# Optimization experiments

Hardware: AMD Instinct MI355X
Metric: run time of the kernel (lower is better)

The kernel has to match this reference:

```python
import jax, jax.numpy as jnp
import numpy as np
from jax.scipy.special import logsumexp

B, T, F = 32, 256, 32   # batch, line width (time), line height (features)
HID = 128
VOCAB = 100             # blank index = VOCAB
LBL = 32                # label length
NEG = -1e30


def _mdlstm(x, Wx, Wh1, Wh2, b):
    # x: [B, H, W, C] -> 2D LSTM: outer scan over width, inner scan over height
    Bb, H, W, C = x.shape
    hid = Wh1.shape[0]

    def col_step(carry, x_col):
        c_left, h_left = carry  # [H, B, hid] states from previous column

        def row_step(rc, inp):
            c_up, h_up = rc          # [B, hid] from previous row
            x_ij, c_l, h_l = inp     # [B, C], [B, hid], [B, hid]
            z = x_ij @ Wx + h_l @ Wh1 + h_up @ Wh2 + b  # [B, 5*hid]
            i_, g_, f1, f2, o_ = jnp.split(z, 5, axis=-1)
            c = jax.nn.sigmoid(f1) * c_l + jax.nn.sigmoid(f2) * c_up + jax.nn.sigmoid(i_) * jnp.tanh(g_)
            h = jax.nn.sigmoid(o_) * jnp.tanh(c)
            return (c, h), (c, h)

        z0 = jnp.zeros((Bb, hid), x.dtype)
        _, (c_col, h_col) = jax.lax.scan(row_step, (z0, z0), (x_col, c_left, h_left))
        return (c_col, h_col), h_col

    x_t = jnp.transpose(x, (2, 1, 0, 3))  # [W, H, B, C]
    zc = jnp.zeros((H, Bb, hid), x.dtype)
    _, hs = jax.lax.scan(col_step, (zc, zc), x_t)  # [W, H, B, hid]
    return jnp.transpose(hs, (2, 1, 0, 3))  # [B, H, W, hid]


def _ctc_loss(logp, labels, blank):
    # logp: [B, T, V] log-softmax; labels: [B, L] int in [0, blank)
    Bb, Tt, V = logp.shape
    Ll = labels.shape[1]
    S = 2 * Ll + 1
    ext = jnp.full((Bb, S), blank, dtype=labels.dtype).at[:, 1::2].set(labels)  # blank-interleaved
    lp_ext = jnp.take_along_axis(logp, jnp.broadcast_to(ext[:, None, :], (Bb, Tt, S)), axis=2)  # [B,T,S]
    prev2 = jnp.concatenate([jnp.full((Bb, 2), blank, dtype=ext.dtype), ext[:, :-2]], axis=1)
    skip = (ext != blank) & (ext != prev2)
    skip = skip.at[:, :2].set(False)
    alpha0 = jnp.full((Bb, S), NEG, logp.dtype).at[:, 0].set(lp_ext[:, 0, 0]).at[:, 1].set(lp_ext[:, 0, 1])

    def step(alpha, lp_t):
        a1 = jnp.concatenate([jnp.full((Bb, 1), NEG, alpha.dtype), alpha[:, :-1]], axis=1)
        a2 = jnp.concatenate([jnp.full((Bb, 2), NEG, alpha.dtype), alpha[:, :-2]], axis=1)
        a2 = jnp.where(skip, a2, NEG)
        new = logsumexp(jnp.stack([alpha, a1, a2], axis=0), axis=0) + lp_t
        return new, None

    alphaT, _ = jax.lax.scan(step, alpha0, jnp.transpose(lp_ext, (1, 0, 2))[1:])
    ll = logsumexp(jnp.stack([alphaT[:, -1], alphaT[:, -2]], axis=0), axis=0)
    return -ll  # [B]


def setup_inputs() -> dict:
    key = jax.random.key(0)
    ks = jax.random.split(key, 8)
    s = 0.08
    return {
        "X": jax.random.normal(ks[0], (B, T, F), jnp.float32),
        "y": jax.random.randint(ks[1], (B, LBL), 0, VOCAB),
        "Wx": jax.random.normal(ks[2], (1, 5 * HID), jnp.float32) * s,
        "Wh1": jax.random.normal(ks[3], (HID, 5 * HID), jnp.float32) * s,
        "Wh2": jax.random.normal(ks[4], (HID, 5 * HID), jnp.float32) * s,
        "b": jax.random.normal(ks[5], (5 * HID,), jnp.float32) * 0.01,
        "W_fc": jax.random.normal(ks[6], (HID, VOCAB + 1), jnp.float32) * s,
        "b_fc": jax.random.normal(ks[7], (VOCAB + 1,), jnp.float32) * 0.01,
    }


def reference(X, y, Wx, Wh1, Wh2, b, W_fc, b_fc):
    x = jnp.transpose(X, (0, 2, 1))[..., None]        # [B, F, T, 1] (image)
    h = _mdlstm(x, Wx, Wh1, Wh2, b)                    # [B, F, T, HID]
    feat = jnp.sum(h, axis=1)                          # collapse over height -> [B, T, HID]
    logits = feat @ W_fc + b_fc                        # [B, T, VOCAB+1]
    logp = jax.nn.log_softmax(logits, axis=-1)
    return _ctc_loss(logp, y, VOCAB)                   # per-example CTC loss [B]
```

## Files before the change

### kernel.cpp

```cpp
#include <hip/hip_runtime.h>

#define NEGF (-1e30f)

typedef __attribute__((ext_vector_type(8))) short short8;
typedef __attribute__((ext_vector_type(4))) float float4v;

template <bool V> struct BC { static constexpr bool value = V; };

__device__ __forceinline__ short f2bf(float f) {
  union { float f; unsigned u; } v; v.f = f;
  unsigned r = v.u + 0x7fffu + ((v.u >> 16) & 1u);
  return (short)(r >> 16);
}
__device__ __forceinline__ float fastrcp(float x) { return __builtin_amdgcn_rcpf(x); }
__device__ __forceinline__ float clamp15(float x) { return fminf(15.0f, fmaxf(-15.0f, x)); }

__global__ void prep_w_kernel(const float* __restrict__ Wh1, const float* __restrict__ Wh2,
                              short* __restrict__ wsW) {
  int t = blockIdx.x * 256 + threadIdx.x;
  int lane = t & 63;
  int frag = t >> 6;
  int nt = frag >> 3, kk = frag & 7;
  int n  = nt * 16 + (lane & 15);
  int kb = kk * 32 + (lane >> 4) * 8;
  short8 v;
#pragma unroll
  for (int j = 0; j < 8; ++j) {
    int k = kb + j;
    float w = (k < 128) ? Wh1[k * 640 + n] : Wh2[(k - 128) * 640 + n];
    v[j] = f2bf(w);
  }
  ((short8*)wsW)[frag * 64 + lane] = v;
}

__global__ __launch_bounds__(512)
void mdlstm_kernel(const float* __restrict__ X, const short* __restrict__ wsW,
                   const float* __restrict__ Wx, const float* __restrict__ bias,
                   float* __restrict__ feat, float* __restrict__ bH0,
                   float* __restrict__ bC0, int* __restrict__ flagA,
                   int* __restrict__ flagB) {
  __shared__ __align__(16) short h_buf[2][17][136];
  __shared__ __align__(16) short wlds[128 * 512];
  __shared__ float featbuf[17][132];

  const int blk  = blockIdx.x;
  const int bat  = blk >> 1;
  const bool isB = blk & 1;
  const int tid  = threadIdx.x;
  const int lane = tid & 63;
  const int g    = tid >> 6;
  const int col  = lane & 15;
  const int quad = lane >> 4;
  const int jj   = g * 16 + col;

  for (int i = tid; i < 2 * 17 * 136 / 2; i += 512) ((int*)h_buf)[i] = 0;
  for (int i = tid; i < 17 * 132; i += 512) ((float*)featbuf)[i] = 0.0f;
  {
    const uint4* src = (const uint4*)(wsW + 192 * 512);
    uint4* dst = (uint4*)wlds;
    for (int i = tid; i < 8192; i += 512) dst[i] = src[i];
  }

  float wx[5], bg[5];
#pragma unroll
  for (int q = 0; q < 5; ++q) {
    wx[q] = Wx[q * 128 + jj];
    bg[q] = bias[q * 128 + jj];
  }
  float cp[4] = {0.f, 0.f, 0.f, 0.f};
  float c15 = 0.0f;
  float pre_h = 0.0f, pre_c = 0.0f;
  float pubH = 0.0f, pubC = 0.0f;
  int knownA = 0;

  const float* Xg = X + bat * 8192;
  float* fb = feat + bat * 32768;
  float* bH = bH0 + bat * 32 * 128;
  float* bC = bC0 + bat * 32 * 128;
  int* fA = flagA + bat;
  int* fB = flagB + bat;
  const short8* W8 = (const short8*)wsW;
  const short8* pW0 = W8 + ((0 * 8 + g) * 8) * 64 + lane;
  const short8* pW1 = W8 + ((1 * 8 + g) * 8) * 64 + lane;
  const short8* pW2 = W8 + ((2 * 8 + g) * 8) * 64 + lane;
  const short8* pL3 = (const short8*)&wlds[((0 * 8 + g) * 8) * 512 + lane * 8];
  const short8* pL4 = (const short8*)&wlds[((1 * 8 + g) * 8) * 512 + lane * 8];
  const int mbase = (isB ? 16 : 0) + quad * 4;
  const int widx0 = (isB ? 1 : 0) + quad * 4;
  const float* pX = Xg - 31 * mbase;
  int sb = 0;
  __syncthreads();

  auto step = [&](int d, auto isb_, auto allv_) {
    constexpr bool IsB = decltype(isb_)::value;
    constexpr bool ALLV = decltype(allv_)::value;
    const int rbuf = (d + 1) & 1, wbuf = d & 1;

    const int wfl = d - (IsB ? 32 : 16);
    if (wfl >= 0 && tid < 128) {
      int fs = sb + 1; if (fs >= 17) fs = 0;
      float v = featbuf[fs][tid];
      featbuf[fs][tid] = 0.0f;
      atomicAdd(&fb[wfl * 128 + tid], v);
    }

    float4v acc[5];
#pragma unroll
    for (int q = 0; q < 5; ++q) acc[q] = (float4v){bg[q], bg[q], bg[q], bg[q]};
    const short8 z8 = (short8){0, 0, 0, 0, 0, 0, 0, 0};
#pragma unroll
    for (int kk = 0; kk < 8; ++kk) {
      const int up = (kk >= 4) ? 1 : 0;
      const int cc = (kk & 3) * 32 + quad * 8;
      int row = col + (IsB ? 1 : 0) - up;
      short8 a0 = (IsB || row >= 0) ? *(const short8*)&h_buf[rbuf][row][cc] : z8;
      short8 b3 = pL3[kk * 64];
      acc[3] = __builtin_amdgcn_mfma_f32_16x16x32_bf16(a0, b3, acc[3], 0, 0, 0);
      short8 b4 = pL4[kk * 64];
      acc[4] = __builtin_amdgcn_mfma_f32_16x16x32_bf16(a0, b4, acc[4], 0, 0, 0);
      short8 b2 = pW2[kk * 64];
      acc[2] = __builtin_amdgcn_mfma_f32_16x16x32_bf16(a0, b2, acc[2], 0, 0, 0);
      short8 b0 = pW0[kk * 64];
      acc[0] = __builtin_amdgcn_mfma_f32_16x16x32_bf16(a0, b0, acc[0], 0, 0, 0);
      short8 b1 = pW1[kk * 64];
      acc[1] = __builtin_amdgcn_mfma_f32_16x16x32_bf16(a0, b1, acc[1], 0, 0, 0);
    }

    float t0 = __shfl_up(cp[3], 16);
    float cu[4];
    cu[0] = quad ? t0 : (IsB ? c15 : 0.0f);
    cu[1] = cp[0]; cu[2] = cp[1]; cu[3] = cp[2];
    const float* pXd = pX + d * 32;
    float xm[4];
#pragma unroll
    for (int r = 0; r < 4; ++r) {
      int w = d - (mbase + r);
      if (ALLV || (w >= 0 && w < 256)) xm[r] = pXd[-31 * r];
    }
#pragma unroll
    for (int r = 0; r < 4; ++r) {
      const int w = d - (mbase + r);
      if (ALLV || (w >= 0 && w < 256)) {
        float c_up = cu[r];
        float c_l  = cp[r];
        float x    = xm[r];
        float zi = clamp15(fmaf(x, wx[0], acc[0][r]));
        float zg = clamp15(fmaf(x, wx[1], acc[1][r]));
        float z1 = clamp15(fmaf(x, wx[2], acc[2][r]));
        float z2 = clamp15(fmaf(x, wx[3], acc[3][r]));
        float zo = clamp15(fmaf(x, wx[4], acc[4][r]));
        float e1 = __expf(z1), e2 = __expf(z2), ei = __expf(zi), eg = __expf(2.0f * zg);
        float A1 = 1.0f + e1, A2 = 1.0f + e2, Ai = 1.0f + ei, G = 1.0f + eg;
        float P = Ai * G, Q = A1 * A2;
        float rD = fastrcp(P * Q);
        float c = (e1 * c_l * (A2 * P) + e2 * c_up * (A1 * P) + ei * (eg - 1.0f) * Q) * rD;
        float eo = __expf(-zo);
        float ec = __expf(2.0f * clamp15(c));
        float h = (ec - 1.0f) * fastrcp((1.0f + eo) * (ec + 1.0f));
        cp[r] = c;
        h_buf[wbuf][widx0 + r][jj] = f2bf(h);
        int s = sb - (quad * 4 + r); if (s < 0) s += 17;
        featbuf[s][jj] += h;
        if (!IsB && r == 3 && quad == 3) {
          pubH = h; pubC = c;
        }
      }
    }
  };

  BC<true> Tv; BC<false> Fv;
  if (!isB) {
    auto aiter = [&](int d, auto allv) {
      if (d >= 16 && quad == 3) {
        const int slot = ((d - 1) & 31) * 128 + jj;
        atomicExch(&bH[slot], pubH);
        atomicExch(&bC[slot], pubC);
      }
      if (d >= 48 && (d & 7) == 0 && lane == 0) {
        while (atomicAdd(fB, 0) < d - 22) {}
      }
      step(d, Fv, allv);
      sb = (sb == 16) ? 0 : sb + 1;
      __syncthreads();
      if ((d & 7) == 0 && d >= 16 && tid == 0) atomicExch(fA, d);
    };
    for (int d = 0; d < 15; ++d)    aiter(d, Fv);
    for (int d = 15; d < 256; ++d)  aiter(d, Tv);
    for (int d = 256; d < 271; ++d) aiter(d, Fv);
    if (quad == 3) {
      const int slot = (270 & 31) * 128 + jj;
      atomicExch(&bH[slot], pubH);
      atomicExch(&bC[slot], pubC);
    }
    if (tid < 128) atomicAdd(&fb[255 * 128 + tid], featbuf[0][tid]);
    __syncthreads();
    if (tid == 0) atomicExch(fA, 272);
  } else {
    {
      if (lane == 0) { while (atomicAdd(fA, 0) < 23) {} knownA = 23; }
      const int slot = 15 * 128 + jj;
      if (quad == 1) pre_h = atomicAdd(&bH[slot], 0.0f);
      else if (quad == 0) pre_c = atomicAdd(&bC[slot], 0.0f);
    }
    auto biter = [&](int e, auto allv) {
      if (quad == 1) h_buf[(e + 1) & 1][0][jj] = f2bf(pre_h);
      else if (quad == 0) c15 = pre_c;
      __syncthreads();
      if ((e & 7) == 7 && tid == 0) atomicExch(fB, e);
      const int ee = e + 1;
      if (ee <= 271) {
        if (lane == 0 && knownA < ee) {
          int tgt = ee + 7; if (tgt > 271) tgt = 271;
          while (atomicAdd(fA, 0) < tgt) {}
          knownA = tgt;
        }
        const int slot = ((ee - 1) & 31) * 128 + jj;
        if (quad == 1) pre_h = atomicAdd(&bH[slot], 0.0f);
        else if (quad == 0) pre_c = atomicAdd(&bC[slot], 0.0f);
      } else {
        pre_h = 0.0f; pre_c = 0.0f;
      }
      step(e, Tv, allv);
      sb = (sb == 16) ? 0 : sb + 1;
    };
    for (int e = 16; e < 31; ++e)   biter(e, Fv);
    for (int e = 31; e < 272; ++e)  biter(e, Tv);
    for (int e = 272; e < 287; ++e) biter(e, Fv);
    __syncthreads();
    if (tid < 128) atomicAdd(&fb[255 * 128 + tid], featbuf[0][tid]);
  }
}

__global__ __launch_bounds__(256)
void logits_kernel(const float* __restrict__ feat, const float* __restrict__ Wfc,
                   const float* __restrict__ bfc, float* __restrict__ logp) {
  __shared__ float sW[128 * 101];
  __shared__ float sF[8][128];
  __shared__ float sL[8][104];
  __shared__ float sLse[8];
  const int tid = threadIdx.x;
  const int b  = blockIdx.x >> 5;
  const int t0 = (blockIdx.x & 31) * 8;

  for (int i = tid; i < 128 * 101; i += 256) sW[i] = Wfc[i];
  for (int i = tid; i < 8 * 128; i += 256)
    sF[i >> 7][i & 127] = feat[(b * 256 + t0 + (i >> 7)) * 128 + (i & 127)];
  __syncthreads();
  for (int idx = tid; idx < 8 * 101; idx += 256) {
    int tr = idx / 101, v = idx - tr * 101;
    float s = bfc[v];
#pragma unroll 4
    for (int k = 0; k < 128; ++k) s += sF[tr][k] * sW[k * 101 + v];
    sL[tr][v] = s;
  }
  __syncthreads();
  if (tid < 8) {
    float m = NEGF;
    for (int v = 0; v < 101; ++v) m = fmaxf(m, sL[tid][v]);
    float su = 0.0f;
    for (int v = 0; v < 101; ++v) su += __expf(sL[tid][v] - m);
    sLse[tid] = m + __logf(su);
  }
  __syncthreads();
  for (int idx = tid; idx < 8 * 101; idx += 256) {
    int tr = idx / 101, v = idx - tr * 101;
    logp[(b * 256 + t0 + tr) * 101 + v] = sL[tr][v] - sLse[tr];
  }
}

__global__ __launch_bounds__(64)
void ctc_kernel(const float* __restrict__ logp, const int* __restrict__ y,
                float* __restrict__ out) {
  const int b = blockIdx.x;
  const int l = threadIdx.x;
  const float* lpb = logp + b * 256 * 101;
  const int* yb = y + b * 32;
  int lab = (l & 1) ? yb[l >> 1] : 100;
  bool skip = (l & 1) && (l >= 3) && (yb[l >> 1] != yb[(l >> 1) - 1]);

  float a   = (l == 0) ? lpb[100] : ((l == 1) ? lpb[lab] : NEGF);
  float a64 = NEGF;
  float pl[4], pb[4];
#pragma unroll
  for (int tt = 0; tt < 4; ++tt) {
    pl[tt] = lpb[(1 + tt) * 101 + lab];
    pb[tt] = lpb[(1 + tt) * 101 + 100];
  }
#pragma unroll 4
  for (int t = 1; t < 256; ++t) {
    const int s = (t - 1) & 3;
    float lpl = pl[s], lpbk = pb[s];
    if (t + 4 < 256) {
      pl[s] = lpb[(t + 4) * 101 + lab];
      pb[s] = lpb[(t + 4) * 101 + 100];
    }
    float am1 = __shfl_up(a, 1); if (l == 0) am1 = NEGF;
    float am2 = __shfl_up(a, 2); if (l < 2 || !skip) am2 = NEGF;
    float m3 = fmaxf(a, fmaxf(am1, am2));
    float na = m3 + __logf(__expf(a - m3) + __expf(am1 - m3) + __expf(am2 - m3)) + lpl;
    float m2 = fmaxf(a64, a);
    float na64 = m2 + __logf(__expf(a64 - m2) + __expf(a - m2)) + lpbk;
    a = na;
    a64 = na64;
  }
  float A63 = __shfl(a, 63);
  float A64 = __shfl(a64, 63);
  if (l == 0) {
    float m = fmaxf(A63, A64);
    out[b] = -(m + __logf(__expf(A63 - m) + __expf(A64 - m)));
  }
}

extern "C" void kernel_launch(void* const* d_in, const int* in_sizes, int n_in,
                              void* d_out, int out_size, void* d_ws, size_t ws_size,
                              hipStream_t stream) {
  const float* X   = (const float*)d_in[0];
  const int*   y   = (const int*)d_in[1];
  const float* Wx  = (const float*)d_in[2];
  const float* Wh1 = (const float*)d_in[3];
  const float* Wh2 = (const float*)d_in[4];
  const float* bi  = (const float*)d_in[5];
  const float* Wfc = (const float*)d_in[6];
  const float* bfc = (const float*)d_in[7];
  float* out = (float*)d_out;

  char* ws = (char*)d_ws;
  short* wsW  = (short*)(ws);
  float* bndH = (float*)(ws + 0x50000);
  float* bndC = (float*)(ws + 0xD0000);
  int*   flgA = (int*)(ws + 0x150000);
  int*   flgB = (int*)(ws + 0x150800);
  float* logp = (float*)(ws + 0x50000);
  float* feat = (float*)(ws + 0x378000);

  hipMemsetAsync(feat, 0, 32 * 256 * 128 * sizeof(float), stream);
  prep_w_kernel<<<80, 256, 0, stream>>>(Wh1, Wh2, wsW);
  mdlstm_kernel<<<64, 512, 0, stream>>>(X, wsW, Wx, bi, feat, bndH, bndC, flgA, flgB);
  logits_kernel<<<1024, 256, 0, stream>>>(feat, Wfc, bfc, logp);
  ctc_kernel<<<32, 64, 0, stream>>>(logp, y, out);
}
```

Before: 867.8 us.

## Halve MDLSTM block to 4 waves, each computing two hidden-unit column groups

The MDLSTM wavefront kernel now runs 256 threads per block instead of 512. Each wave handles two 16-wide hidden-unit groups, sharing one A-fragment load across 10 MFMAs per k-step and making barriers cheaper. In exchange each wave does twice the gate math serially and needs more registers. The latency-bound recurrence could get shorter or longer per step. The clamp is also switched to a single fmed3 instruction.

```diff
diff --git a/kernel.cpp b/kernel.cpp
--- a/kernel.cpp
+++ b/kernel.cpp
@@ -13,7 +13,7 @@
   return (short)(r >> 16);
 }
 __device__ __forceinline__ float fastrcp(float x) { return __builtin_amdgcn_rcpf(x); }
-__device__ __forceinline__ float clamp15(float x) { return fminf(15.0f, fmaxf(-15.0f, x)); }
+__device__ __forceinline__ float clamp15(float x) { return __builtin_amdgcn_fmed3f(x, -15.0f, 15.0f); }
 
 __global__ void prep_w_kernel(const float* __restrict__ Wh1, const float* __restrict__ Wh2,
                               short* __restrict__ wsW) {
@@ -33,7 +33,7 @@
   ((short8*)wsW)[frag * 64 + lane] = v;
 }
 
-__global__ __launch_bounds__(512)
+__global__ __launch_bounds__(256)
 void mdlstm_kernel(const float* __restrict__ X, const short* __restrict__ wsW,
                    const float* __restrict__ Wx, const float* __restrict__ bias,
                    float* __restrict__ feat, float* __restrict__ bH0,
@@ -48,29 +48,34 @@
   const bool isB = blk & 1;
   const int tid  = threadIdx.x;
   const int lane = tid & 63;
-  const int g    = tid >> 6;
+  const int wv   = tid >> 6;
   const int col  = lane & 15;
   const int quad = lane >> 4;
-  const int jj   = g * 16 + col;
-
-  for (int i = tid; i < 2 * 17 * 136 / 2; i += 512) ((int*)h_buf)[i] = 0;
-  for (int i = tid; i < 17 * 132; i += 512) ((float*)featbuf)[i] = 0.0f;
+
+  for (int i = tid; i < 2 * 17 * 136 / 2; i += 256) ((int*)h_buf)[i] = 0;
+  for (int i = tid; i < 17 * 132; i += 256) ((float*)featbuf)[i] = 0.0f;
   {
     const uint4* src = (const uint4*)(wsW + 192 * 512);
     uint4* dst = (uint4*)wlds;
-    for (int i = tid; i < 8192; i += 512) dst[i] = src[i];
-  }
-
-  float wx[5], bg[5];
-#pragma unroll
-  for (int q = 0; q < 5; ++q) {
-    wx[q] = Wx[q * 128 + jj];
-    bg[q] = bias[q * 128 + jj];
-  }
-  float cp[4] = {0.f, 0.f, 0.f, 0.f};
-  float c15 = 0.0f;
-  float pre_h = 0.0f, pre_c = 0.0f;
-  float pubH = 0.0f, pubC = 0.0f;
+    for (int i = tid; i < 8192; i += 256) dst[i] = src[i];
+  }
+
+  int jjs[2];
+  float wx[2][5], bg[2][5];
+#pragma unroll
+  for (int s = 0; s < 2; ++s) {
+    const int g = wv * 2 + s;
+    jjs[s] = g * 16 + col;
+#pragma unroll
+    for (int q = 0; q < 5; ++q) {
+      wx[s][q] = Wx[q * 128 + jjs[s]];
+      bg[s][q] = bias[q * 128 + jjs[s]];
+    }
+  }
+  float cp[2][4] = {{0.f,0.f,0.f,0.f},{0.f,0.f,0.f,0.f}};
+  float c15[2] = {0.f, 0.f};
+  float pre_h[2] = {0.f, 0.f}, pre_c[2] = {0.f, 0.f};
+  float pubH[2] = {0.f, 0.f}, pubC[2] = {0.f, 0.f};
   int knownA = 0;
 
   const float* Xg = X + bat * 8192;
@@ -80,11 +85,16 @@
   int* fA = flagA + bat;
   int* fB = flagB + bat;
   const short8* W8 = (const short8*)wsW;
-  const short8* pW0 = W8 + ((0 * 8 + g) * 8) * 64 + lane;
-  const short8* pW1 = W8 + ((1 * 8 + g) * 8) * 64 + lane;
-  const short8* pW2 = W8 + ((2 * 8 + g) * 8) * 64 + lane;
-  const short8* pL3 = (const short8*)&wlds[((0 * 8 + g) * 8) * 512 + lane * 8];
-  const short8* pL4 = (const short8*)&wlds[((1 * 8 + g) * 8) * 512 + lane * 8];
+  const short8* pW0[2], *pW1[2], *pW2[2], *pL3[2], *pL4[2];
+#pragma unroll
+  for (int s = 0; s < 2; ++s) {
+    const int g = wv * 2 + s;
+    pW0[s] = W8 + ((0 * 8 + g) * 8) * 64 + lane;
+    pW1[s] = W8 + ((1 * 8 + g) * 8) * 64 + lane;
+    pW2[s] = W8 + ((2 * 8 + g) * 8) * 64 + lane;
+    pL3[s] = (const short8*)&wlds[((0 * 8 + g) * 8) * 512 + lane * 8];
+    pL4[s] = (const short8*)&wlds[((1 * 8 + g) * 8) * 512 + lane * 8];
+  }
   const int mbase = (isB ? 16 : 0) + quad * 4;
   const int widx0 = (isB ? 1 : 0) + quad * 4;
   const float* pX = Xg - 31 * mbase;
@@ -104,9 +114,12 @@
       atomicAdd(&fb[wfl * 128 + tid], v);
     }
 
-    float4v acc[5];
-#pragma unroll
-    for (int q = 0; q < 5; ++q) acc[q] = (float4v){bg[q], bg[q], bg[q], bg[q]};
+    float4v acc[2][5];
+#pragma unroll
+    for (int s = 0; s < 2; ++s)
+#pragma unroll
+      for (int q = 0; q < 5; ++q)
+        acc[s][q] = (float4v){bg[s][q], bg[s][q], bg[s][q], bg[s][q]};
     const short8 z8 = (short8){0, 0, 0, 0, 0, 0, 0, 0};
 #pragma unroll
     for (int kk = 0; kk < 8; ++kk) {
@@ -114,22 +127,28 @@
       const int cc = (kk & 3) * 32 + quad * 8;
       int row = col + (IsB ? 1 : 0) - up;
       short8 a0 = (IsB || row >= 0) ? *(const short8*)&h_buf[rbuf][row][cc] : z8;
-      short8 b3 = pL3[kk * 64];
-      acc[3] = __builtin_amdgcn_mfma_f32_16x16x32_bf16(a0, b3, acc[3], 0, 0, 0);
-      short8 b4 = pL4[kk * 64];
-      acc[4] = __builtin_amdgcn_mfma_f32_16x16x32_bf16(a0, b4, acc[4], 0, 0, 0);
-      short8 b2 = pW2[kk * 64];
-      acc[2] = __builtin_amdgcn_mfma_f32_16x16x32_bf16(a0, b2, acc[2], 0, 0, 0);
-      short8 b0 = pW0[kk * 64];
-      acc[0] = __builtin_amdgcn_mfma_f32_16x16x32_bf16(a0, b0, acc[0], 0, 0, 0);
-      short8 b1 = pW1[kk * 64];
-      acc[1] = __builtin_amdgcn_mfma_f32_16x16x32_bf16(a0, b1, acc[1], 0, 0, 0);
-    }
-
-    float t0 = __shfl_up(cp[3], 16);
-    float cu[4];
-    cu[0] = quad ? t0 : (IsB ? c15 : 0.0f);
-    cu[1] = cp[0]; cu[2] = cp[1]; cu[3] = cp[2];
+#pragma unroll
+      for (int s = 0; s < 2; ++s) {
+        short8 b3 = pL3[s][kk * 64];
+        acc[s][3] = __builtin_amdgcn_mfma_f32_16x16x32_bf16(a0, b3, acc[s][3], 0, 0, 0);
+        short8 b4 = pL4[s][kk * 64];
+        acc[s][4] = __builtin_amdgcn_mfma_f32_16x16x32_bf16(a0, b4, acc[s][4], 0, 0, 0);
+        short8 b2 = pW2[s][kk * 64];
+        acc[s][2] = __builtin_amdgcn_mfma_f32_16x16x32_bf16(a0, b2, acc[s][2], 0, 0, 0);
+        short8 b0 = pW0[s][kk * 64];
+        acc[s][0] = __builtin_amdgcn_mfma_f32_16x16x32_bf16(a0, b0, acc[s][0], 0, 0, 0);
+        short8 b1 = pW1[s][kk * 64];
+        acc[s][1] = __builtin_amdgcn_mfma_f32_16x16x32_bf16(a0, b1, acc[s][1], 0, 0, 0);
+      }
+    }
+
+    float cu[2][4];
+#pragma unroll
+    for (int s = 0; s < 2; ++s) {
+      float t0 = __shfl_up(cp[s][3], 16);
+      cu[s][0] = quad ? t0 : (IsB ? c15[s] : 0.0f);
+      cu[s][1] = cp[s][0]; cu[s][2] = cp[s][1]; cu[s][3] = cp[s][2];
+    }
     const float* pXd = pX + d * 32;
     float xm[4];
 #pragma unroll
@@ -138,31 +157,35 @@
       if (ALLV || (w >= 0 && w < 256)) xm[r] = pXd[-31 * r];
     }
 #pragma unroll
-    for (int r = 0; r < 4; ++r) {
-      const int w = d - (mbase + r);
-      if (ALLV || (w >= 0 && w < 256)) {
-        float c_up = cu[r];
-        float c_l  = cp[r];
-        float x    = xm[r];
-        float zi = clamp15(fmaf(x, wx[0], acc[0][r]));
-        float zg = clamp15(fmaf(x, wx[1], acc[1][r]));
-        float z1 = clamp15(fmaf(x, wx[2], acc[2][r]));
-        float z2 = clamp15(fmaf(x, wx[3], acc[3][r]));
-        float zo = clamp15(fmaf(x, wx[4], acc[4][r]));
-        float e1 = __expf(z1), e2 = __expf(z2), ei = __expf(zi), eg = __expf(2.0f * zg);
-        float A1 = 1.0f + e1, A2 = 1.0f + e2, Ai = 1.0f + ei, G = 1.0f + eg;
-        float P = Ai * G, Q = A1 * A2;
-        float rD = fastrcp(P * Q);
-        float c = (e1 * c_l * (A2 * P) + e2 * c_up * (A1 * P) + ei * (eg - 1.0f) * Q) * rD;
-        float eo = __expf(-zo);
-        float ec = __expf(2.0f * clamp15(c));
-        float h = (ec - 1.0f) * fastrcp((1.0f + eo) * (ec + 1.0f));
-        cp[r] = c;
-        h_buf[wbuf][widx0 + r][jj] = f2bf(h);
-        int s = sb - (quad * 4 + r); if (s < 0) s += 17;
-        featbuf[s][jj] += h;
-        if (!IsB && r == 3 && quad == 3) {
-          pubH = h; pubC = c;
+    for (int s = 0; s < 2; ++s) {
+      const int jj = jjs[s];
+#pragma unroll
+      for (int r = 0; r < 4; ++r) {
+        const int w = d - (mbase + r);
+        if (ALLV || (w >= 0 && w < 256)) {
+          float c_up = cu[s][r];
+          float c_l  = cp[s][r];
+          float x    = xm[r];
+          float zi = clamp15(fmaf(x, wx[s][0], acc[s][0][r]));
+          float zg = clamp15(fmaf(x, wx[s][1], acc[s][1][r]));
+          float z1 = clamp15(fmaf(x, wx[s][2], acc[s][2][r]));
+          float z2 = clamp15(fmaf(x, wx[s][3], acc[s][3][r]));
+          float zo = clamp15(fmaf(x, wx[s][4], acc[s][4][r]));
+          float e1 = __expf(z1), e2 = __expf(z2), ei = __expf(zi), eg = __expf(2.0f * zg);
+          float A1 = 1.0f + e1, A2 = 1.0f + e2, Ai = 1.0f + ei, G = 1.0f + eg;
+          float P = Ai * G, Q = A1 * A2;
+          float rD = fastrcp(P * Q);
+          float c = (e1 * c_l * (A2 * P) + e2 * c_up * (A1 * P) + ei * (eg - 1.0f) * Q) * rD;
+          float eo = __expf(-zo);
+          float ec = __expf(2.0f * clamp15(c));
+          float h = (ec - 1.0f) * fastrcp((1.0f + eo) * (ec + 1.0f));
+          cp[s][r] = c;
+          h_buf[wbuf][widx0 + r][jj] = f2bf(h);
+          int sl = sb - (quad * 4 + r); if (sl < 0) sl += 17;
+          featbuf[sl][jj] += h;
+          if (!IsB && r == 3 && quad == 3) {
+            pubH[s] = h; pubC[s] = c;
+          }
         }
       }
     }
@@ -172,9 +195,12 @@
   if (!isB) {
     auto aiter = [&](int d, auto allv) {
       if (d >= 16 && quad == 3) {
-        const int slot = ((d - 1) & 31) * 128 + jj;
-        atomicExch(&bH[slot], pubH);
-        atomicExch(&bC[slot], pubC);
+#pragma unroll
+        for (int s = 0; s < 2; ++s) {
+          const int slot = ((d - 1) & 31) * 128 + jjs[s];
+          atomicExch(&bH[slot], pubH[s]);
+          atomicExch(&bC[slot], pubC[s]);
+        }
       }
       if (d >= 48 && (d & 7) == 0 && lane == 0) {
         while (atomicAdd(fB, 0) < d - 22) {}
@@ -188,9 +214,12 @@
     for (int d = 15; d < 256; ++d)  aiter(d, Tv);
     for (int d = 256; d < 271; ++d) aiter(d, Fv);
     if (quad == 3) {
-      const int slot = (270 & 31) * 128 + jj;
-      atomicExch(&bH[slot], pubH);
-      atomicExch(&bC[slot], pubC);
+#pragma unroll
+      for (int s = 0; s < 2; ++s) {
+        const int slot = (270 & 31) * 128 + jjs[s];
+        atomicExch(&bH[slot], pubH[s]);
+        atomicExch(&bC[slot], pubC[s]);
+      }
     }
     if (tid < 128) atomicAdd(&fb[255 * 128 + tid], featbuf[0][tid]);
     __syncthreads();
@@ -198,13 +227,19 @@
   } else {
     {
       if (lane == 0) { while (atomicAdd(fA, 0) < 23) {} knownA = 23; }
-      const int slot = 15 * 128 + jj;
-      if (quad == 1) pre_h = atomicAdd(&bH[slot], 0.0f);
-      else if (quad == 0) pre_c = atomicAdd(&bC[slot], 0.0f);
+#pragma unroll
+      for (int s = 0; s < 2; ++s) {
+        const int slot = 15 * 128 + jjs[s];
+        if (quad == 1) pre_h[s] = atomicAdd(&bH[slot], 0.0f);
+        else if (quad == 0) pre_c[s] = atomicAdd(&bC[slot], 0.0f);
+      }
     }
     auto biter = [&](int e, auto allv) {
-      if (quad == 1) h_buf[(e + 1) & 1][0][jj] = f2bf(pre_h);
-      else if (quad == 0) c15 = pre_c;
+#pragma unroll
+      for (int s = 0; s < 2; ++s) {
+        if (quad == 1) h_buf[(e + 1) & 1][0][jjs[s]] = f2bf(pre_h[s]);
+        else if (quad == 0) c15[s] = pre_c[s];
+      }
       __syncthreads();
       if ((e & 7) == 7 && tid == 0) atomicExch(fB, e);
       const int ee = e + 1;
@@ -214,11 +249,14 @@
           while (atomicAdd(fA, 0) < tgt) {}
           knownA = tgt;
         }
-        const int slot = ((ee - 1) & 31) * 128 + jj;
-        if (quad == 1) pre_h = atomicAdd(&bH[slot], 0.0f);
-        else if (quad == 0) pre_c = atomicAdd(&bC[slot], 0.0f);
+#pragma unroll
+        for (int s = 0; s < 2; ++s) {
+          const int slot = ((ee - 1) & 31) * 128 + jjs[s];
+          if (quad == 1) pre_h[s] = atomicAdd(&bH[slot], 0.0f);
+          else if (quad == 0) pre_c[s] = atomicAdd(&bC[slot], 0.0f);
+        }
       } else {
-        pre_h = 0.0f; pre_c = 0.0f;
+        pre_h[0] = pre_h[1] = 0.0f; pre_c[0] = pre_c[1] = 0.0f;
       }
       step(e, Tv, allv);
       sb = (sb == 16) ? 0 : sb + 1;
@@ -335,7 +373,7 @@
 
   hipMemsetAsync(feat, 0, 32 * 256 * 128 * sizeof(float), stream);
   prep_w_kernel<<<80, 256, 0, stream>>>(Wh1, Wh2, wsW);
-  mdlstm_kernel<<<64, 512, 0, stream>>>(X, wsW, Wx, bi, feat, bndH, bndC, flgA, flgB);
+  mdlstm_kernel<<<64, 256, 0, stream>>>(X, wsW, Wx, bi, feat, bndH, bndC, flgA, flgB);
   logits_kernel<<<1024, 256, 0, stream>>>(feat, Wfc, bfc, logp);
   ctc_kernel<<<32, 64, 0, stream>>>(logp, y, out);
 }
```

Result: slower. 1.352 ms (+55.8%).
